# Kernel optimization log

Measured on AMD Instinct MI355X. Metric: run time of the kernel, lower is better.

The kernel has to match this reference:

```python
import jax, jax.numpy as jnp
import numpy as np

USR_NUM = 100000
D_IN = 32
D_HID = 32
D_MID = 16
D_OUT = 2
N_EDGES = 1600000
EPS = 1e-16  # matches torch_geometric.utils.softmax denominator eps


def _glorot(key, shape):
    fan_in, fan_out = shape[0], shape[1]
    lim = np.sqrt(6.0 / (fan_in + fan_out))
    return jax.random.uniform(key, shape, jnp.float32, -lim, lim)


def setup_inputs() -> dict:
    key = jax.random.key(0)
    ks = jax.random.split(key, 16)
    inp = {
        "edge_index": jax.random.randint(ks[0], (2, N_EDGES), 0, USR_NUM, dtype=jnp.int64)
        if jax.config.jax_enable_x64 else jax.random.randint(ks[0], (2, N_EDGES), 0, USR_NUM).astype(jnp.int32),
        "emb": jax.random.normal(ks[1], (USR_NUM, D_IN), jnp.float32),
        # conv1: TransformerConv(32 -> 32, heads=1)
        "Wq1": _glorot(ks[2], (D_IN, D_HID)), "bq1": jnp.zeros((D_HID,), jnp.float32),
        "Wk1": _glorot(ks[3], (D_IN, D_HID)), "bk1": jnp.zeros((D_HID,), jnp.float32),
        "Wv1": _glorot(ks[4], (D_IN, D_HID)), "bv1": jnp.zeros((D_HID,), jnp.float32),
        "Ws1": _glorot(ks[5], (D_IN, D_HID)), "bs1": jnp.zeros((D_HID,), jnp.float32),
        # conv2: TransformerConv(32 -> 16, heads=1)
        "Wq2": _glorot(ks[6], (D_HID, D_MID)), "bq2": jnp.zeros((D_MID,), jnp.float32),
        "Wk2": _glorot(ks[7], (D_HID, D_MID)), "bk2": jnp.zeros((D_MID,), jnp.float32),
        "Wv2": _glorot(ks[8], (D_HID, D_MID)), "bv2": jnp.zeros((D_MID,), jnp.float32),
        "Ws2": _glorot(ks[9], (D_HID, D_MID)), "bs2": jnp.zeros((D_MID,), jnp.float32),
        # output: Linear(16 -> 2)
        "Wo": _glorot(ks[10], (D_MID, D_OUT)), "bo": jnp.zeros((D_OUT,), jnp.float32),
    }
    return inp


def transformer_conv(x, src, dst, Wq, bq, Wk, bk, Wv, bv, Ws, bs, n_nodes):
    # edge (j=src -> i=dst): alpha_ij = softmax_i( <q_i, k_j> / sqrt(d) )
    d = Wq.shape[1]
    q = (x @ Wq + bq)[dst]          # [E, d]
    k = (x @ Wk + bk)[src]          # [E, d]
    v = (x @ Wv + bv)[src]          # [E, d]
    alpha = jnp.sum(q * k, axis=-1) / jnp.sqrt(jnp.float32(d))  # [E]
    # segment softmax over incoming edges of each destination node
    seg_max = jax.ops.segment_max(alpha, dst, num_segments=n_nodes)  # [N]
    e = jnp.exp(alpha - seg_max[dst])
    seg_sum = jax.ops.segment_sum(e, dst, num_segments=n_nodes)      # [N]
    w = e / (seg_sum[dst] + EPS)
    agg = jax.ops.segment_sum(v * w[:, None], dst, num_segments=n_nodes)  # [N, d]
    return agg + x @ Ws + bs  # root/skip connection (PyG default root_weight=True)


def reference(edge_index, emb,
              Wq1, bq1, Wk1, bk1, Wv1, bv1, Ws1, bs1,
              Wq2, bq2, Wk2, bk2, Wv2, bv2, Ws2, bs2,
              Wo, bo):
    src, dst = edge_index[0], edge_index[1]
    h = transformer_conv(emb, src, dst, Wq1, bq1, Wk1, bk1, Wv1, bv1, Ws1, bs1, USR_NUM)
    h = jax.nn.relu(h)
    h = transformer_conv(h, src, dst, Wq2, bq2, Wk2, bk2, Wv2, bv2, Ws2, bs2, USR_NUM)
    h = jax.nn.relu(h)
    return h @ Wo + bo  # [N, 2]
```

## Files before the change

### kernel.cpp

```cpp
#include <hip/hip_runtime.h>
#include <hip/hip_bf16.h>

typedef __hip_bfloat16 bf16;
typedef unsigned int uint;
typedef unsigned short ushort;

#define N_NODES 100000
#define N_EDGES_C 1600000
#define NSB2 392
#define NSB2P 512
#define RND 2048
#define EPB (RND / 256)
#define NBIN 64
#define G_RAD ((N_EDGES_C + RND - 1) / RND)
#define HCAP 5632
#define NSLOT (NSB2 * 256)
#define NCHUNK 16
#define KEYN (256 * NCHUNK)

__device__ __forceinline__ float ldf(const void* p, long i, int isbf) {
    return isbf ? __bfloat162float(((const bf16*)p)[i]) : ((const float*)p)[i];
}
__device__ __forceinline__ int ldidx(const int* ei, long pos, int is64) {
    return is64 ? ei[2 * pos] : ei[pos];
}
__device__ __forceinline__ ushort bfb(float x) {
    bf16 h = __float2bfloat16(x);
    return *(ushort*)&h;
}
__device__ __forceinline__ float bl(uint u) { return __uint_as_float(u << 16); }
__device__ __forceinline__ float bh(uint u) { return __uint_as_float(u & 0xFFFF0000u); }

__global__ void setup_kernel(
    const void* emb, const int* ei,
    const void* Wq1, const void* bq1, const void* Wk1, const void* bk1,
    const void* Wv1, const void* bv1, const void* Ws1, const void* bs1,
    const void* Wq2, const void* bq2, const void* Wk2, const void* bk2,
    const void* Wv2, const void* bv2, const void* Ws2, const void* bs2,
    const void* Wo, const void* bo,
    int* flags, float* wp1, float* bp1, float* wp2, float* bp2, float* woF,
    int* curSB) {
    __shared__ int sf0;
    int t = threadIdx.x;
    if (t < 64) {
        const bf16* pb = (const bf16*)emb;
        int bad = 0;
        for (int i = t; i < 256; i += 64) {
            float v = __bfloat162float(pb[i]);
            if (!(v > -1.0e6f && v < 1.0e6f)) bad++;
        }
        int nz = 0;
        for (int i = 2 * t + 1; i < 256; i += 128) nz += (ei[i] != 0) ? 1 : 0;
#pragma unroll
        for (int m = 32; m >= 1; m >>= 1) {
            bad += __shfl_xor(bad, m, 64);
            nz  += __shfl_xor(nz, m, 64);
        }
        if (t == 0) {
            int f0 = (bad <= 8) ? 1 : 0;
            flags[0] = f0;
            flags[1] = (nz == 0) ? 1 : 0;
            sf0 = f0;
        }
    }
    __syncthreads();
    int isbf = sf0;
    for (int i = t; i < 1024; i += 256) {
        wp1[i]        = ldf(Wq1, i, isbf);
        wp1[1024 + i] = ldf(Wk1, i, isbf);
        wp1[2048 + i] = ldf(Wv1, i, isbf);
        wp1[3072 + i] = ldf(Ws1, i, isbf);
    }
    for (int i = t; i < 512; i += 256) {
        wp2[i]        = ldf(Wq2, i, isbf);
        wp2[512 + i]  = ldf(Wk2, i, isbf);
        wp2[1024 + i] = ldf(Wv2, i, isbf);
        wp2[1536 + i] = ldf(Ws2, i, isbf);
    }
    if (t < 32) {
        bp1[t] = ldf(bq1, t, isbf); bp1[32 + t] = ldf(bk1, t, isbf);
        bp1[64 + t] = ldf(bv1, t, isbf); bp1[96 + t] = ldf(bs1, t, isbf);
        woF[t] = ldf(Wo, t, isbf);
    }
    if (t < 16) {
        bp2[t] = ldf(bq2, t, isbf); bp2[16 + t] = ldf(bk2, t, isbf);
        bp2[32 + t] = ldf(bv2, t, isbf); bp2[48 + t] = ldf(bs2, t, isbf);
    }
    if (t < 2) woF[32 + t] = ldf(bo, t, isbf);
    curSB[t] = 0; curSB[t + 256] = 0;
}

template <int DOUT, bool RUNTIME_DTYPE>
__device__ __forceinline__ void node_linear_body(
    const void* __restrict__ X, const float* __restrict__ wpack,
    const float* __restrict__ bpack, const int* __restrict__ flags,
    float* __restrict__ q, ushort* __restrict__ kvb, float* __restrict__ s,
    int bid, float* __restrict__ sW, float* __restrict__ sbias, float* __restrict__ sX) {
    const int TPN = DOUT / 4;
    const int NPB = 256 / TPN;
    const int W_ELEMS = 4 * 32 * DOUT;

    const float4* wp4 = (const float4*)wpack;
    float4* sW4 = (float4*)sW;
    for (int i = threadIdx.x; i < W_ELEMS / 4; i += 256) sW4[i] = wp4[i];
    if (threadIdx.x < 4 * DOUT) sbias[threadIdx.x] = bpack[threadIdx.x];
    const int base = bid * NPB * 32;
    bool useBf = RUNTIME_DTYPE && (flags[0] != 0);
    if (useBf) {
        for (int i = threadIdx.x; i < NPB * 32; i += 256) {
            int g = base + i;
            float xv = (g < N_NODES * 32) ? __bfloat162float(((const bf16*)X)[g]) : 0.0f;
            sX[(i >> 5) * 36 + (i & 31)] = xv;
        }
    } else {
        for (int i = threadIdx.x; i < NPB * 32; i += 256) {
            int g = base + i;
            sX[(i >> 5) * 36 + (i & 31)] = (g < N_NODES * 32) ? ((const float*)X)[g] : 0.0f;
        }
    }
    __syncthreads();

    int l = threadIdx.x / TPN;
    int c4 = (threadIdx.x % TPN) * 4;
    int n = bid * NPB + l;
    if (n >= N_NODES) return;

    float xr[32];
#pragma unroll
    for (int j = 0; j < 8; j++) {
        float4 t4 = *(const float4*)&sX[l * 36 + 4 * j];
        xr[4 * j] = t4.x; xr[4 * j + 1] = t4.y; xr[4 * j + 2] = t4.z; xr[4 * j + 3] = t4.w;
    }
    float acc[4][4];
#pragma unroll
    for (int m = 0; m < 4; m++)
#pragma unroll
        for (int j = 0; j < 4; j++) acc[m][j] = sbias[m * DOUT + c4 + j];

#pragma unroll
    for (int t = 0; t < 32; t++) {
#pragma unroll
        for (int m = 0; m < 4; m++) {
            float4 w = *(const float4*)&sW[(m * 32 + t) * DOUT + c4];
            acc[m][0] += xr[t] * w.x;
            acc[m][1] += xr[t] * w.y;
            acc[m][2] += xr[t] * w.z;
            acc[m][3] += xr[t] * w.w;
        }
    }
    size_t o = (size_t)n * DOUT + c4;
    *(float4*)&q[o] = make_float4(acc[0][0], acc[0][1], acc[0][2], acc[0][3]);
    *(float4*)&s[o] = make_float4(acc[3][0], acc[3][1], acc[3][2], acc[3][3]);
    size_t okv = (size_t)n * 2 * DOUT + c4;
    ushort4 kp = make_ushort4(bfb(acc[1][0]), bfb(acc[1][1]), bfb(acc[1][2]), bfb(acc[1][3]));
    ushort4 vp = make_ushort4(bfb(acc[2][0]), bfb(acc[2][1]), bfb(acc[2][2]), bfb(acc[2][3]));
    *(ushort4*)&kvb[okv]        = kp;
    *(ushort4*)&kvb[okv + DOUT] = vp;
}

struct RadixS {
    int cnt[NSB2P]; int excl[NSB2P]; int part[256]; int gbase[NSB2P];
    uint sVal[RND]; ushort sSb[RND];
};
struct LinS { float sW[4096]; float sbias[128]; float sX[32 * 36]; };
union alignas(16) FusedS { RadixS r; LinS l; };

__global__ void __launch_bounds__(256, 4) fused_ra_nl(
    const int* __restrict__ ei, const int* __restrict__ flags,
    int* __restrict__ curSB, uint* __restrict__ pairsSB,
    const void* __restrict__ X, const float* __restrict__ wpack,
    const float* __restrict__ bpack,
    float* __restrict__ q, ushort* __restrict__ kvb, float* __restrict__ s) {
    __shared__ FusedS u;
    if (blockIdx.x >= G_RAD) {
        node_linear_body<32, true>(X, wpack, bpack, flags, q, kvb, s,
                                   (int)blockIdx.x - G_RAD, u.l.sW, u.l.sbias, u.l.sX);
        return;
    }
    int* cnt = u.r.cnt; int* excl = u.r.excl; int* part = u.r.part; int* gbase = u.r.gbase;
    uint* sVal = u.r.sVal; ushort* sSb = u.r.sSb;
    const int is64 = flags[1];
    int t = threadIdx.x;
    cnt[t] = 0; cnt[t + 256] = 0;
    __syncthreads();
    long base = (long)blockIdx.x * RND;

    int mySb[EPB]; int myRank[EPB]; uint myPk[EPB];
#pragma unroll
    for (int r = 0; r < EPB; r++) {
        long e = base + r * 256 + t;
        mySb[r] = -1;
        if (e < N_EDGES_C) {
            int d = ldidx(ei, (long)N_EDGES_C + e, is64);
            int src = ldidx(ei, e, is64);
            int sb = d >> 8;
            myPk[r] = (uint)src | ((uint)(d & 255) << 17);
            myRank[r] = atomicAdd(&cnt[sb], 1);
            mySb[r] = sb;
        }
    }
    __syncthreads();
    int v0 = cnt[2 * t], v1 = cnt[2 * t + 1];
    int sum2 = v0 + v1;
    part[t] = sum2;
    __syncthreads();
    for (int off = 1; off < 256; off <<= 1) {
        int u2 = (t >= off) ? part[t - off] : 0;
        __syncthreads();
        part[t] += u2;
        __syncthreads();
    }
    int basex = part[t] - sum2;
    excl[2 * t]     = basex;
    excl[2 * t + 1] = basex + v0;
    __syncthreads();
#pragma unroll
    for (int r = 0; r < EPB; r++) {
        if (mySb[r] >= 0) {
            int pos = excl[mySb[r]] + myRank[r];
            sVal[pos] = myPk[r];
            sSb[pos] = (ushort)mySb[r];
        }
    }
    for (int i = t; i < NSB2P; i += 256)
        gbase[i] = (cnt[i] > 0) ? atomicAdd(&curSB[i], cnt[i]) : 0;
    __syncthreads();
    int tot = excl[NSB2P - 1] + cnt[NSB2P - 1];
    for (int i = t; i < tot; i += 256) {
        int sb = sSb[i];
        int gp = gbase[sb] + (i - excl[sb]);
        if (gp < HCAP)
            pairsSB[(size_t)sb * HCAP + gp] = sVal[i];
    }
}

__global__ void __launch_bounds__(256, 2) radix_b(
    const int* __restrict__ curSB, const uint* __restrict__ pairsSB,
    int* __restrict__ esrc,
    int* __restrict__ rowbeg, int* __restrict__ rowend,
    int* __restrict__ perm) {
    __shared__ uint sP[HCAP];
    __shared__ int dcnt[KEYN];
    __shared__ int dexcl[KEYN];
    __shared__ int dcur[KEYN];
    __shared__ int part[256];
    __shared__ int hbin[NBIN], hbase[NBIN], hcur[NBIN];
    int sbh = blockIdx.x;
    int t = threadIdx.x;
    int n = min(curSB[sbh], HCAP);
    for (int i = t; i < KEYN; i += 256) { dcnt[i] = 0; dcur[i] = 0; }
    if (t < NBIN) { hbin[t] = 0; hcur[t] = 0; }
    perm[sbh * 256 + t] = -1;
    __syncthreads();
    const uint* srcp = pairsSB + (size_t)sbh * HCAP;
    for (int i = t; i < n; i += 256) {
        uint pk = srcp[i];
        sP[i] = pk;
        int key = (int)((pk >> 17) & 255) * NCHUNK + (int)((pk & 0x1FFFFu) >> 13);
        atomicAdd(&dcnt[key], 1);
    }
    __syncthreads();
    const int kb = t * NCHUNK;
    int sum = 0;
#pragma unroll
    for (int j = 0; j < NCHUNK; j++) sum += dcnt[kb + j];
    int v = sum;
    part[t] = v;
    __syncthreads();
    for (int off = 1; off < 256; off <<= 1) {
        int u2 = (t >= off) ? part[t - off] : 0;
        __syncthreads();
        part[t] += u2;
        __syncthreads();
    }
    int run = part[t] - v;
    int myExcl = run;
#pragma unroll
    for (int j = 0; j < NCHUNK; j++) { dexcl[kb + j] = run; run += dcnt[kb + j]; }
    __syncthreads();
    const int EB = sbh * HCAP;
    int dst = sbh * 256 + t;
    int mybin = -1;
    if (dst < N_NODES) {
        rowbeg[dst] = EB + min(myExcl, HCAP);
        rowend[dst] = EB + min(myExcl + v, HCAP);
        mybin = min(v, NBIN - 1);
        atomicAdd(&hbin[mybin], 1);
    }
    __syncthreads();
    if (t < 64) {
        int hv = hbin[t];
        int sfx = hv;
#pragma unroll
        for (int off = 1; off < 64; off <<= 1) {
            int u2 = __shfl_down(sfx, off, 64);
            if (t + off < 64) sfx += u2;
        }
        hbase[t] = sfx - hv;
    }
    __syncthreads();
    if (dst < N_NODES) {
        int r = atomicAdd(&hcur[mybin], 1);
        perm[sbh * 256 + hbase[mybin] + r] = dst;
    }
    for (int i = t; i < n; i += 256) {
        uint pk = sP[i];
        int key = (int)((pk >> 17) & 255) * NCHUNK + (int)((pk & 0x1FFFFu) >> 13);
        int p2 = dexcl[key] + atomicAdd(&dcur[key], 1);
        if (p2 < HCAP) esrc[EB + p2] = (int)(pk & 0x1FFFF);
    }
}

template <int D, bool LAYER2>
__global__ void gather_attn(const int* __restrict__ perm,
                            const int* __restrict__ rowbeg, const int* __restrict__ rowend,
                            const int* __restrict__ esrc,
                            const float* __restrict__ q, const ushort* __restrict__ kvb,
                            const float* __restrict__ s,
                            const float* __restrict__ wp2,
                            const float* __restrict__ bp2,
                            const float* __restrict__ woF,
                            const int* __restrict__ flags,
                            float* __restrict__ q2o, ushort* __restrict__ kvb2o,
                            float* __restrict__ s2o,
                            void* __restrict__ out) {
    const int LPD = D / 8;
    const int G = 64 / LPD;
    const int WPC = 256 / G;
    __shared__ float sW2[2048];
    __shared__ float sb2[64];
    __shared__ float sH[64 * 36];
    __shared__ int sDst[64];

    if constexpr (!LAYER2) {
        for (int i = threadIdx.x; i < 2048; i += 256) sW2[i] = wp2[i];
        if (threadIdx.x < 64) sb2[threadIdx.x] = bp2[threadIdx.x];
    }

    int lane = threadIdx.x & 63;
    int W = (blockIdx.x * blockDim.x + threadIdx.x) >> 6;
    int g = lane / LPD;
    int c = lane % LPD;
    int chunkc = W / WPC;
    int window = ((W % WPC) * 5) % WPC;
    int idx = chunkc * 256 + window * G + g;
    int dst = perm[idx];
    if constexpr (LAYER2) {
        if (dst < 0) return;
    }
    bool alive = (dst >= 0);

    const float rsq = (D == 32) ? 0.17677669529663689f : 0.25f;
    float4 qa = make_float4(0.f, 0.f, 0.f, 0.f), qb = qa;
    int beg = 0, end = 0;
    if (alive) {
        qa = *(const float4*)(q + (size_t)dst * D + 8 * c);
        qb = *(const float4*)(q + (size_t)dst * D + 8 * c + 4);
        beg = rowbeg[dst]; end = rowend[dst];
    }

    const char* kvbase = (const char*)kvb;
    const int ROW = 4 * D;
    const int koff = 16 * c;
    const int voff = 2 * D + 16 * c;

    float sum0 = 0.f, sum1 = 0.f;
    float a0[8] = {0,0,0,0,0,0,0,0};
    float a1[8] = {0,0,0,0,0,0,0,0};

    uint4 kq[4], vq[4];
#pragma unroll
    for (int r = 0; r < 4; r++) {
        int sn = (beg + r < end) ? esrc[beg + r] : 0;
        const char* p = kvbase + (size_t)sn * ROW;
        kq[r] = *(const uint4*)(p + koff);
        vq[r] = *(const uint4*)(p + voff);
    }

    for (int e = beg; e < end; e += 4) {
        uint4 kc[4], vc[4];
#pragma unroll
        for (int r = 0; r < 4; r++) { kc[r] = kq[r]; vc[r] = vq[r]; }
#pragma unroll
        for (int r = 0; r < 4; r++) {
            if (e + 4 + r < end) {
                const char* p = kvbase + (size_t)esrc[e + 4 + r] * ROW;
                kq[r] = *(const uint4*)(p + koff);
                vq[r] = *(const uint4*)(p + voff);
            }
        }
#pragma unroll
        for (int r = 0; r < 4; r++) {
            if (e + r < end) {
                uint4 kA = kc[r], vA = vc[r];
                float pd = qa.x * bl(kA.x) + qa.y * bh(kA.x) + qa.z * bl(kA.y) + qa.w * bh(kA.y)
                         + qb.x * bl(kA.z) + qb.y * bh(kA.z) + qb.z * bl(kA.w) + qb.w * bh(kA.w);
#pragma unroll
                for (int m = LPD / 2; m >= 1; m >>= 1) pd += __shfl_xor(pd, m, LPD);
                float ex = __expf(fminf(fmaxf(pd * rsq, -80.0f), 80.0f));
                if (r & 1) {
                    sum1 += ex;
                    a1[0] += bl(vA.x) * ex; a1[1] += bh(vA.x) * ex;
                    a1[2] += bl(vA.y) * ex; a1[3] += bh(vA.y) * ex;
                    a1[4] += bl(vA.z) * ex; a1[5] += bh(vA.z) * ex;
                    a1[6] += bl(vA.w) * ex; a1[7] += bh(vA.w) * ex;
                } else {
                    sum0 += ex;
                    a0[0] += bl(vA.x) * ex; a0[1] += bh(vA.x) * ex;
                    a0[2] += bl(vA.y) * ex; a0[3] += bh(vA.y) * ex;
                    a0[4] += bl(vA.z) * ex; a0[5] += bh(vA.z) * ex;
                    a0[6] += bl(vA.w) * ex; a0[7] += bh(vA.w) * ex;
                }
            }
        }
    }
    float inv = 1.0f / (sum0 + sum1 + 1e-16f);
    float4 sa = make_float4(0.f, 0.f, 0.f, 0.f), sbv = sa;
    if (alive) {
        sa  = *(const float4*)(s + (size_t)dst * D + 8 * c);
        sbv = *(const float4*)(s + (size_t)dst * D + 8 * c + 4);
    }
    float h[8];
    h[0] = (a0[0] + a1[0]) * inv + sa.x;  h[1] = (a0[1] + a1[1]) * inv + sa.y;
    h[2] = (a0[2] + a1[2]) * inv + sa.z;  h[3] = (a0[3] + a1[3]) * inv + sa.w;
    h[4] = (a0[4] + a1[4]) * inv + sbv.x; h[5] = (a0[5] + a1[5]) * inv + sbv.y;
    h[6] = (a0[6] + a1[6]) * inv + sbv.z; h[7] = (a0[7] + a1[7]) * inv + sbv.w;
#pragma unroll
    for (int j = 0; j < 8; j++) h[j] = h[j] > 0.0f ? h[j] : 0.0f;

    if constexpr (!LAYER2) {
        int gl = (threadIdx.x >> 6) * G + g;
        if (alive) {
            *(float4*)&sH[gl * 36 + 8 * c]     = make_float4(h[0], h[1], h[2], h[3]);
            *(float4*)&sH[gl * 36 + 8 * c + 4] = make_float4(h[4], h[5], h[6], h[7]);
        }
        if (c == 0) sDst[gl] = dst;
        __syncthreads();
        int l = threadIdx.x >> 2;
        int c4 = (threadIdx.x & 3) * 4;
        int nd = sDst[l];
        if (nd >= 0) {
            float acc2[4][4];
#pragma unroll
            for (int m = 0; m < 4; m++)
#pragma unroll
                for (int j = 0; j < 4; j++) acc2[m][j] = sb2[m * 16 + c4 + j];
#pragma unroll
            for (int t2 = 0; t2 < 32; t2++) {
                float xv = sH[l * 36 + t2];
#pragma unroll
                for (int m = 0; m < 4; m++) {
                    float4 w = *(const float4*)&sW2[(m * 32 + t2) * 16 + c4];
                    acc2[m][0] += xv * w.x;
                    acc2[m][1] += xv * w.y;
                    acc2[m][2] += xv * w.z;
                    acc2[m][3] += xv * w.w;
                }
            }
            size_t o = (size_t)nd * 16 + c4;
            *(float4*)&q2o[o] = make_float4(acc2[0][0], acc2[0][1], acc2[0][2], acc2[0][3]);
            *(float4*)&s2o[o] = make_float4(acc2[3][0], acc2[3][1], acc2[3][2], acc2[3][3]);
            size_t okv = (size_t)nd * 32 + c4;
            ushort4 kp = make_ushort4(bfb(acc2[1][0]), bfb(acc2[1][1]), bfb(acc2[1][2]), bfb(acc2[1][3]));
            ushort4 vp = make_ushort4(bfb(acc2[2][0]), bfb(acc2[2][1]), bfb(acc2[2][2]), bfb(acc2[2][3]));
            *(ushort4*)&kvb2o[okv]      = kp;
            *(ushort4*)&kvb2o[okv + 16] = vp;
        }
    } else {
        float p0 = 0.f, p1 = 0.f;
#pragma unroll
        for (int j = 0; j < 8; j++) {
            p0 += h[j] * woF[(8 * c + j) * 2 + 0];
            p1 += h[j] * woF[(8 * c + j) * 2 + 1];
        }
#pragma unroll
        for (int m = LPD / 2; m >= 1; m >>= 1) {
            p0 += __shfl_xor(p0, m, LPD);
            p1 += __shfl_xor(p1, m, LPD);
        }
        if (c == 0) {
            float o0 = p0 + woF[32];
            float o1 = p1 + woF[33];
            if (flags[0]) {
                ((bf16*)out)[dst * 2 + 0] = __float2bfloat16(o0);
                ((bf16*)out)[dst * 2 + 1] = __float2bfloat16(o1);
            } else {
                ((float*)out)[dst * 2 + 0] = o0;
                ((float*)out)[dst * 2 + 1] = o1;
            }
        }
    }
}

extern "C" void kernel_launch(void* const* d_in, const int* in_sizes, int n_in,
                              void* d_out, int out_size, void* d_ws, size_t ws_size,
                              hipStream_t stream) {
    const int* ei  = (const int*)d_in[0];
    const void* emb = d_in[1];
    const void *Wq1 = d_in[2],  *bq1 = d_in[3];
    const void *Wk1 = d_in[4],  *bk1 = d_in[5];
    const void *Wv1 = d_in[6],  *bv1 = d_in[7];
    const void *Ws1 = d_in[8],  *bs1 = d_in[9];
    const void *Wq2 = d_in[10], *bq2 = d_in[11];
    const void *Wk2 = d_in[12], *bk2 = d_in[13];
    const void *Wv2 = d_in[14], *bv2 = d_in[15];
    const void *Ws2 = d_in[16], *bs2 = d_in[17];
    const void *Wo  = d_in[18], *bo  = d_in[19];

    const size_t ND   = (size_t)N_NODES * 32;
    const size_t ND16 = (size_t)N_NODES * 16;
    const size_t SBTOT = (size_t)NSB2 * HCAP;
    float* base   = (float*)d_ws;
    int*   flags  = (int*)base;
    float* wp1    = base + 64;
    float* bp1    = wp1 + 4096;
    float* wp2    = bp1 + 128;
    float* bp2    = wp2 + 2048;
    float* woF    = bp2 + 64;
    int*   curSB  = (int*)(woF + 64);
    int*   rowbeg = curSB + 512;
    int*   rowend = rowbeg + N_NODES;
    int*   perm   = rowend + N_NODES;
    float* p      = (float*)(perm + NSLOT);
    float* q      = p; p += ND;
    float* s      = p; p += ND;
    ushort* kvb   = (ushort*)p; p += ND;
    float* q2     = p; p += ND16;
    float* s2     = p; p += ND16;
    ushort* kvb2  = (ushort*)p; p += ND16;
    int*   esrc   = (int*)p; p += SBTOT;
    uint*  pairsSB = (uint*)p;

    const int B = 256;
    const int gNL32  = (N_NODES + 31) / 32;
    const int gFused = G_RAD + gNL32;
    const int gG1    = NSLOT / 64;
    const int gG2    = NSLOT / 128;

    setup_kernel<<<1, B, 0, stream>>>(emb, ei,
        Wq1, bq1, Wk1, bk1, Wv1, bv1, Ws1, bs1,
        Wq2, bq2, Wk2, bk2, Wv2, bv2, Ws2, bs2, Wo, bo,
        flags, wp1, bp1, wp2, bp2, woF, curSB);

    fused_ra_nl<<<gFused, B, 0, stream>>>(ei, flags, curSB, pairsSB,
                                          emb, wp1, bp1, q, kvb, s);

    radix_b<<<NSB2, B, 0, stream>>>(curSB, pairsSB, esrc, rowbeg, rowend, perm);

    gather_attn<32, false><<<gG1, B, 0, stream>>>(
        perm, rowbeg, rowend, esrc, q, kvb, s, wp2, bp2, nullptr, flags,
        q2, kvb2, s2, nullptr);

    gather_attn<16, true><<<gG2, B, 0, stream>>>(
        perm, rowbeg, rowend, esrc, q2, kvb2, s2, nullptr, nullptr, woF, flags,
        nullptr, nullptr, nullptr, d_out);
}
```

Before: 260.7 us.

## Split each node's edges across two lane groups and use wave-shuffle block scans

In the gather-attention kernels, each destination node now gets two lane groups that take alternating edges. Their partial softmax sums and weighted value accumulators are combined with cross-lane shuffles, which doubles the edge-level parallelism and memory-level parallelism per node at the cost of halving nodes per block. The node-permutation window remapping is dropped and launch bounds are added to allow higher occupancy. Both radix kernels replace the shared-memory Hillis-Steele scan, which needed many block barriers, with a wavefront shuffle scan plus a small per-wave sum array.

```diff
diff --git a/kernel.cpp b/kernel.cpp
--- a/kernel.cpp
+++ b/kernel.cpp
@@ -159,7 +159,7 @@
 }
 
 struct RadixS {
-    int cnt[NSB2P]; int excl[NSB2P]; int part[256]; int gbase[NSB2P];
+    int cnt[NSB2P]; int excl[NSB2P]; int gbase[NSB2P]; int wsum[4];
     uint sVal[RND]; ushort sSb[RND];
 };
 struct LinS { float sW[4096]; float sbias[128]; float sX[32 * 36]; };
@@ -177,7 +177,7 @@
                                    (int)blockIdx.x - G_RAD, u.l.sW, u.l.sbias, u.l.sX);
         return;
     }
-    int* cnt = u.r.cnt; int* excl = u.r.excl; int* part = u.r.part; int* gbase = u.r.gbase;
+    int* cnt = u.r.cnt; int* excl = u.r.excl; int* gbase = u.r.gbase;
     uint* sVal = u.r.sVal; ushort* sSb = u.r.sSb;
     const int is64 = flags[1];
     int t = threadIdx.x;
@@ -202,15 +202,19 @@
     __syncthreads();
     int v0 = cnt[2 * t], v1 = cnt[2 * t + 1];
     int sum2 = v0 + v1;
-    part[t] = sum2;
-    __syncthreads();
-    for (int off = 1; off < 256; off <<= 1) {
-        int u2 = (t >= off) ? part[t - off] : 0;
-        __syncthreads();
-        part[t] += u2;
-        __syncthreads();
-    }
-    int basex = part[t] - sum2;
+    int lane6 = t & 63, wid6 = t >> 6;
+    int x = sum2;
+#pragma unroll
+    for (int off = 1; off < 64; off <<= 1) {
+        int u2 = __shfl_up(x, off, 64);
+        if (lane6 >= off) x += u2;
+    }
+    if (lane6 == 63) u.r.wsum[wid6] = x;
+    __syncthreads();
+    int wbase = 0;
+#pragma unroll
+    for (int w = 0; w < 4; w++) if (w < wid6) wbase += u.r.wsum[w];
+    int basex = wbase + x - sum2;
     excl[2 * t]     = basex;
     excl[2 * t + 1] = basex + v0;
     __syncthreads();
@@ -243,7 +247,7 @@
     __shared__ int dcnt[KEYN];
     __shared__ int dexcl[KEYN];
     __shared__ int dcur[KEYN];
-    __shared__ int part[256];
+    __shared__ int wsum[4];
     __shared__ int hbin[NBIN], hbase[NBIN], hcur[NBIN];
     int sbh = blockIdx.x;
     int t = threadIdx.x;
@@ -265,16 +269,20 @@
 #pragma unroll
     for (int j = 0; j < NCHUNK; j++) sum += dcnt[kb + j];
     int v = sum;
-    part[t] = v;
-    __syncthreads();
-    for (int off = 1; off < 256; off <<= 1) {
-        int u2 = (t >= off) ? part[t - off] : 0;
-        __syncthreads();
-        part[t] += u2;
-        __syncthreads();
-    }
-    int run = part[t] - v;
-    int myExcl = run;
+    int lane6 = t & 63, wid6 = t >> 6;
+    int x = v;
+#pragma unroll
+    for (int off = 1; off < 64; off <<= 1) {
+        int u2 = __shfl_up(x, off, 64);
+        if (lane6 >= off) x += u2;
+    }
+    if (lane6 == 63) wsum[wid6] = x;
+    __syncthreads();
+    int wbase = 0;
+#pragma unroll
+    for (int w = 0; w < 4; w++) if (w < wid6) wbase += wsum[w];
+    int myExcl = wbase + x - v;
+    int run = myExcl;
 #pragma unroll
     for (int j = 0; j < NCHUNK; j++) { dexcl[kb + j] = run; run += dcnt[kb + j]; }
     __syncthreads();
@@ -312,7 +320,8 @@
 }
 
 template <int D, bool LAYER2>
-__global__ void gather_attn(const int* __restrict__ perm,
+__global__ void __launch_bounds__(256, 8) gather_attn(
+                            const int* __restrict__ perm,
                             const int* __restrict__ rowbeg, const int* __restrict__ rowend,
                             const int* __restrict__ esrc,
                             const float* __restrict__ q, const ushort* __restrict__ kvb,
@@ -325,12 +334,12 @@
                             float* __restrict__ s2o,
                             void* __restrict__ out) {
     const int LPD = D / 8;
-    const int G = 64 / LPD;
-    const int WPC = 256 / G;
-    __shared__ float sW2[2048];
-    __shared__ float sb2[64];
-    __shared__ float sH[64 * 36];
-    __shared__ int sDst[64];
+    const int LG  = 2 * LPD;
+    const int G   = 64 / LG;
+    __shared__ float sW2[LAYER2 ? 4 : 2048];
+    __shared__ float sb2[LAYER2 ? 4 : 64];
+    __shared__ float sH[LAYER2 ? 4 : 32 * 36];
+    __shared__ int sDst[LAYER2 ? 4 : 32];
 
     if constexpr (!LAYER2) {
         for (int i = threadIdx.x; i < 2048; i += 256) sW2[i] = wp2[i];
@@ -339,11 +348,11 @@
 
     int lane = threadIdx.x & 63;
     int W = (blockIdx.x * blockDim.x + threadIdx.x) >> 6;
-    int g = lane / LPD;
-    int c = lane % LPD;
-    int chunkc = W / WPC;
-    int window = ((W % WPC) * 5) % WPC;
-    int idx = chunkc * 256 + window * G + g;
+    int g = lane / LG;
+    int sub = lane % LG;
+    int c = sub % LPD;
+    int eh = sub / LPD;
+    int idx = W * G + g;
     int dst = perm[idx];
     if constexpr (LAYER2) {
         if (dst < 0) return;
@@ -368,30 +377,33 @@
     float a0[8] = {0,0,0,0,0,0,0,0};
     float a1[8] = {0,0,0,0,0,0,0,0};
 
+    int ebase = beg + eh;
     uint4 kq[4], vq[4];
 #pragma unroll
     for (int r = 0; r < 4; r++) {
-        int sn = (beg + r < end) ? esrc[beg + r] : 0;
+        int pos = ebase + 2 * r;
+        int sn = (pos < end) ? esrc[pos] : 0;
         const char* p = kvbase + (size_t)sn * ROW;
         kq[r] = *(const uint4*)(p + koff);
         vq[r] = *(const uint4*)(p + voff);
     }
 
-    for (int e = beg; e < end; e += 4) {
+    for (int e = ebase; e < end; e += 8) {
         uint4 kc[4], vc[4];
 #pragma unroll
         for (int r = 0; r < 4; r++) { kc[r] = kq[r]; vc[r] = vq[r]; }
 #pragma unroll
         for (int r = 0; r < 4; r++) {
-            if (e + 4 + r < end) {
-                const char* p = kvbase + (size_t)esrc[e + 4 + r] * ROW;
+            int pos = e + 8 + 2 * r;
+            if (pos < end) {
+                const char* p = kvbase + (size_t)esrc[pos] * ROW;
                 kq[r] = *(const uint4*)(p + koff);
                 vq[r] = *(const uint4*)(p + voff);
             }
         }
 #pragma unroll
         for (int r = 0; r < 4; r++) {
-            if (e + r < end) {
+            if (e + 2 * r < end) {
                 uint4 kA = kc[r], vA = vc[r];
                 float pd = qa.x * bl(kA.x) + qa.y * bh(kA.x) + qa.z * bl(kA.y) + qa.w * bh(kA.y)
                          + qb.x * bl(kA.z) + qb.y * bh(kA.z) + qb.z * bl(kA.w) + qb.w * bh(kA.w);
@@ -414,57 +426,67 @@
             }
         }
     }
-    float inv = 1.0f / (sum0 + sum1 + 1e-16f);
+    float sT = sum0 + sum1;
+    sT += __shfl_xor(sT, LPD, LG);
+    float aT[8];
+#pragma unroll
+    for (int j = 0; j < 8; j++) {
+        aT[j] = a0[j] + a1[j];
+        aT[j] += __shfl_xor(aT[j], LPD, LG);
+    }
+    float inv = 1.0f / (sT + 1e-16f);
     float4 sa = make_float4(0.f, 0.f, 0.f, 0.f), sbv = sa;
     if (alive) {
         sa  = *(const float4*)(s + (size_t)dst * D + 8 * c);
         sbv = *(const float4*)(s + (size_t)dst * D + 8 * c + 4);
     }
     float h[8];
-    h[0] = (a0[0] + a1[0]) * inv + sa.x;  h[1] = (a0[1] + a1[1]) * inv + sa.y;
-    h[2] = (a0[2] + a1[2]) * inv + sa.z;  h[3] = (a0[3] + a1[3]) * inv + sa.w;
-    h[4] = (a0[4] + a1[4]) * inv + sbv.x; h[5] = (a0[5] + a1[5]) * inv + sbv.y;
-    h[6] = (a0[6] + a1[6]) * inv + sbv.z; h[7] = (a0[7] + a1[7]) * inv + sbv.w;
+    h[0] = aT[0] * inv + sa.x;  h[1] = aT[1] * inv + sa.y;
+    h[2] = aT[2] * inv + sa.z;  h[3] = aT[3] * inv + sa.w;
+    h[4] = aT[4] * inv + sbv.x; h[5] = aT[5] * inv + sbv.y;
+    h[6] = aT[6] * inv + sbv.z; h[7] = aT[7] * inv + sbv.w;
 #pragma unroll
     for (int j = 0; j < 8; j++) h[j] = h[j] > 0.0f ? h[j] : 0.0f;
 
     if constexpr (!LAYER2) {
         int gl = (threadIdx.x >> 6) * G + g;
-        if (alive) {
+        if (alive && eh == 0) {
             *(float4*)&sH[gl * 36 + 8 * c]     = make_float4(h[0], h[1], h[2], h[3]);
             *(float4*)&sH[gl * 36 + 8 * c + 4] = make_float4(h[4], h[5], h[6], h[7]);
         }
-        if (c == 0) sDst[gl] = dst;
+        if (c == 0 && eh == 0) sDst[gl] = dst;
         __syncthreads();
-        int l = threadIdx.x >> 2;
-        int c4 = (threadIdx.x & 3) * 4;
-        int nd = sDst[l];
-        if (nd >= 0) {
-            float acc2[4][4];
-#pragma unroll
-            for (int m = 0; m < 4; m++)
-#pragma unroll
-                for (int j = 0; j < 4; j++) acc2[m][j] = sb2[m * 16 + c4 + j];
-#pragma unroll
-            for (int t2 = 0; t2 < 32; t2++) {
-                float xv = sH[l * 36 + t2];
-#pragma unroll
-                for (int m = 0; m < 4; m++) {
-                    float4 w = *(const float4*)&sW2[(m * 32 + t2) * 16 + c4];
-                    acc2[m][0] += xv * w.x;
-                    acc2[m][1] += xv * w.y;
-                    acc2[m][2] += xv * w.z;
-                    acc2[m][3] += xv * w.w;
+        if (threadIdx.x < 128) {
+            int l = threadIdx.x >> 2;
+            int c4 = (threadIdx.x & 3) * 4;
+            int nd = sDst[l];
+            if (nd >= 0) {
+                float acc2[4][4];
+#pragma unroll
+                for (int m = 0; m < 4; m++)
+#pragma unroll
+                    for (int j = 0; j < 4; j++) acc2[m][j] = sb2[m * 16 + c4 + j];
+#pragma unroll
+                for (int t2 = 0; t2 < 32; t2++) {
+                    float xv = sH[l * 36 + t2];
+#pragma unroll
+                    for (int m = 0; m < 4; m++) {
+                        float4 w = *(const float4*)&sW2[(m * 32 + t2) * 16 + c4];
+                        acc2[m][0] += xv * w.x;
+                        acc2[m][1] += xv * w.y;
+                        acc2[m][2] += xv * w.z;
+                        acc2[m][3] += xv * w.w;
+                    }
                 }
+                size_t o = (size_t)nd * 16 + c4;
+                *(float4*)&q2o[o] = make_float4(acc2[0][0], acc2[0][1], acc2[0][2], acc2[0][3]);
+                *(float4*)&s2o[o] = make_float4(acc2[3][0], acc2[3][1], acc2[3][2], acc2[3][3]);
+                size_t okv = (size_t)nd * 32 + c4;
+                ushort4 kp = make_ushort4(bfb(acc2[1][0]), bfb(acc2[1][1]), bfb(acc2[1][2]), bfb(acc2[1][3]));
+                ushort4 vp = make_ushort4(bfb(acc2[2][0]), bfb(acc2[2][1]), bfb(acc2[2][2]), bfb(acc2[2][3]));
+                *(ushort4*)&kvb2o[okv]      = kp;
+                *(ushort4*)&kvb2o[okv + 16] = vp;
             }
-            size_t o = (size_t)nd * 16 + c4;
-            *(float4*)&q2o[o] = make_float4(acc2[0][0], acc2[0][1], acc2[0][2], acc2[0][3]);
-            *(float4*)&s2o[o] = make_float4(acc2[3][0], acc2[3][1], acc2[3][2], acc2[3][3]);
-            size_t okv = (size_t)nd * 32 + c4;
-            ushort4 kp = make_ushort4(bfb(acc2[1][0]), bfb(acc2[1][1]), bfb(acc2[1][2]), bfb(acc2[1][3]));
-            ushort4 vp = make_ushort4(bfb(acc2[2][0]), bfb(acc2[2][1]), bfb(acc2[2][2]), bfb(acc2[2][3]));
-            *(ushort4*)&kvb2o[okv]      = kp;
-            *(ushort4*)&kvb2o[okv + 16] = vp;
         }
     } else {
         float p0 = 0.f, p1 = 0.f;
@@ -478,7 +500,7 @@
             p0 += __shfl_xor(p0, m, LPD);
             p1 += __shfl_xor(p1, m, LPD);
         }
-        if (c == 0) {
+        if (c == 0 && eh == 0) {
             float o0 = p0 + woF[32];
             float o1 = p1 + woF[33];
             if (flags[0]) {
@@ -534,8 +556,8 @@
     const int B = 256;
     const int gNL32  = (N_NODES + 31) / 32;
     const int gFused = G_RAD + gNL32;
-    const int gG1    = NSLOT / 64;
-    const int gG2    = NSLOT / 128;
+    const int gG1    = NSLOT / 8 / 4;
+    const int gG2    = NSLOT / 16 / 4;
 
     setup_kernel<<<1, B, 0, stream>>>(emb, ei,
         Wq1, bq1, Wk1, bk1, Wv1, bv1, Ws1, bs1,
```

Measured after the change: 524.6 us. +101.2%, slower.
